# Performance work log

Measured on AMD Instinct MI355X. Metric: run time of the kernel, lower is better.

Reference implementation:

```python
import jax, jax.numpy as jnp
import numpy as np

B, H, S, D = 8, 32, 1024, 128
MAX_LEN = 2048
CACHE_POS = 128  # tokens already resident in cache (memory tokens)


def setup_inputs() -> dict:
    key = jax.random.key(0)
    k1, k2, k3, k4, k5 = jax.random.split(key, 5)
    return {
        "query_states": jax.random.normal(k1, (B, H, S, D), dtype=jnp.float32),
        "key_states": jax.random.normal(k2, (B, H, S, D), dtype=jnp.float32),
        "value_states": jax.random.normal(k3, (B, H, S, D), dtype=jnp.float32),
        "key_cache": jax.random.normal(k4, (B, H, MAX_LEN, D), dtype=jnp.float32),
        "value_cache": jax.random.normal(k5, (B, H, MAX_LEN, D), dtype=jnp.float32),
        "cache_position": CACHE_POS,
    }


def reference(query_states, key_states, value_states, key_cache, value_cache, cache_position):
    # --- HymbaCache.update_cache ---
    seq_len = key_states.shape[2]
    end_pos = cache_position + seq_len  # == sliding_window + num_memory_tokens, no shift needed
    key_cache = jax.lax.dynamic_update_slice(key_cache, key_states, (0, 0, cache_position, 0))
    value_cache = jax.lax.dynamic_update_slice(value_cache, value_states, (0, 0, cache_position, 0))
    k = key_cache[:, :, :end_pos]    # [B,H,end_pos,D]
    v = value_cache[:, :, :end_pos]  # [B,H,end_pos,D]
    # --- scaled dot-product attention over cached K/V ---
    scale = 1.0 / jnp.sqrt(jnp.asarray(k.shape[-1], dtype=query_states.dtype))
    scores = jnp.einsum('bhqd,bhkd->bhqk', query_states, k) * scale
    attn = jax.nn.softmax(scores, axis=-1)
    out = jnp.einsum('bhqk,bhkd->bhqd', attn, v)
    return out
```

## Files before the change

### kernel.cpp

```cpp
#include <hip/hip_runtime.h>
#include <hip/hip_bf16.h>
#include <stdint.h>

constexpr int Bb = 8, Hh = 32, Ss = 1024, Dd = 128, ML = 2048;
constexpr int CACHE_POS_C = 128;
constexpr int QT = 128;
constexpr int KT = 32;
constexpr int NTT = (CACHE_POS_C + Ss) / KT;
constexpr int PSTR = 40;

typedef __attribute__((ext_vector_type(8))) short bf16x8;
typedef __attribute__((ext_vector_type(4))) float f32x4;
typedef __attribute__((ext_vector_type(4))) unsigned u32x4;

__device__ __forceinline__ short f2bf(float x) {
    __hip_bfloat16 h = __float2bfloat16(x);
    return __builtin_bit_cast(short, h);
}

__device__ __forceinline__ float fast_exp2(float x) {
#if __has_builtin(__builtin_amdgcn_exp2f)
    return __builtin_amdgcn_exp2f(x);
#else
    return exp2f(x);
#endif
}

__device__ __forceinline__ void gll16(const void* g, void* l) {
    __builtin_amdgcn_global_load_lds(
        (const __attribute__((address_space(1))) unsigned int*)(uintptr_t)g,
        (__attribute__((address_space(3))) unsigned int*)(uintptr_t)l,
        16, 0, 0);
}

__global__ __launch_bounds__(256)
void prepack(const float* __restrict__ KN, const float* __restrict__ VN,
             const float* __restrict__ KC, const float* __restrict__ VC,
             const int* __restrict__ CPOS, short* __restrict__ KP,
             short* __restrict__ VP)
{
    const int blk = blockIdx.x;
    const int bh  = blk / NTT;
    const int t   = blk - bh * NTT;
    const int cpos = CPOS[0];
    const int endp = cpos + Ss;

    #pragma unroll
    for (int r = 0; r < 2; ++r) {
        const int c  = r * 256 + threadIdx.x;
        const int kk = c >> 7, h = (c >> 6) & 1, l = c & 63;
        const int row = t * KT + 2 * (l & 15) + h;
        const int d0  = kk * 32 + (l >> 4) * 8;
        bf16x8 o;
        if (row < endp) {
            const float* src = (row < cpos)
                ? KC + ((size_t)bh * ML + row) * Dd + d0
                : KN + ((size_t)bh * Ss + (row - cpos)) * Dd + d0;
            float4 a = ((const float4*)src)[0];
            float4 b = ((const float4*)src)[1];
            o[0] = f2bf(a.x); o[1] = f2bf(a.y); o[2] = f2bf(a.z); o[3] = f2bf(a.w);
            o[4] = f2bf(b.x); o[5] = f2bf(b.y); o[6] = f2bf(b.z); o[7] = f2bf(b.w);
        } else {
            #pragma unroll
            for (int j = 0; j < 8; ++j) o[j] = 0;
        }
        *(bf16x8*)(&KP[((size_t)blk * 512 + c) * 8]) = o;
    }
    #pragma unroll
    for (int r = 0; r < 2; ++r) {
        const int c  = r * 256 + threadIdx.x;
        const int tt = c >> 6, l = c & 63;
        const int d   = tt * 16 + (l & 15);
        const int kv0 = t * KT + (l >> 4) * 8;
        bf16x8 o;
        #pragma unroll
        for (int j = 0; j < 8; ++j) {
            const int row = kv0 + j;
            float x = 0.f;
            if (row < endp) {
                x = (row < cpos) ? VC[((size_t)bh * ML + row) * Dd + d]
                                 : VN[((size_t)bh * Ss + (row - cpos)) * Dd + d];
            }
            o[j] = f2bf(x);
        }
        *(bf16x8*)(&VP[((size_t)blk * 512 + c) * 8]) = o;
    }
}

__global__ __launch_bounds__(256, 3)
void attn_main(const float* __restrict__ Q, const short* __restrict__ KP,
               const short* __restrict__ VP, const int* __restrict__ CPOS,
               float* __restrict__ OUT)
{
    __shared__ __align__(16) short Kl[2][4096];
    __shared__ __align__(16) short Vl[2][4096];

    const int tid = threadIdx.x;
    const int wv  = tid >> 6;
    const int l64 = tid & 63;
    const int g   = l64 >> 4;
    const int ln  = l64 & 15;

    const int bid = blockIdx.x;
    const int bh  = ((bid & 7) << 5) | (bid >> 6);
    const int qt  = (bid >> 3) & 7;
    const int q0w = qt * QT + wv * 32;

    const int cpos = CPOS[0];
    const int endp = cpos + Ss;
    int ntile = (endp + KT - 1) / KT;
    if (ntile > NTT) ntile = NTT;
    const float nInv = (float)(ntile * KT - endp);

    const float SCALE2 = 0.08838834764831845f * 1.44269504088896340736f;

    bf16x8 qf[2][4];
    #pragma unroll
    for (int rb = 0; rb < 2; ++rb) {
        const float* qr = Q + ((size_t)bh * Ss + q0w + rb * 16 + ln) * Dd + g * 8;
        #pragma unroll
        for (int kk = 0; kk < 4; ++kk) {
            float4 a = *(const float4*)(qr + kk * 32);
            float4 b = *(const float4*)(qr + kk * 32 + 4);
            bf16x8 f;
            f[0] = f2bf(a.x * SCALE2); f[1] = f2bf(a.y * SCALE2);
            f[2] = f2bf(a.z * SCALE2); f[3] = f2bf(a.w * SCALE2);
            f[4] = f2bf(b.x * SCALE2); f[5] = f2bf(b.y * SCALE2);
            f[6] = f2bf(b.z * SCALE2); f[7] = f2bf(b.w * SCALE2);
            qf[rb][kk] = f;
        }
    }

    f32x4 O[2][8];
    #pragma unroll
    for (int rb = 0; rb < 2; ++rb)
        #pragma unroll
        for (int t = 0; t < 8; ++t) O[rb][t] = (f32x4){0.f, 0.f, 0.f, 0.f};
    f32x4 Lacc[2];
    Lacc[0] = (f32x4){0.f, 0.f, 0.f, 0.f};
    Lacc[1] = (f32x4){0.f, 0.f, 0.f, 0.f};

    const f32x4 ZZ = (f32x4){0.f, 0.f, 0.f, 0.f};

    bf16x8 ones;
    #pragma unroll
    for (int j = 0; j < 8; ++j) ones[j] = (short)0x3F80;

    const size_t kbase = (size_t)bh * NTT * 4096;

    #pragma unroll
    for (int r = 0; r < 2; ++r) {
        const int ch = r * 256 + tid;
        gll16(KP + kbase + (size_t)ch * 8, &Kl[0][(r * 256 + wv * 64) * 8]);
        gll16(VP + kbase + (size_t)ch * 8, &Vl[0][(r * 256 + wv * 64) * 8]);
    }
    __syncthreads();

    int cur = 0;
    for (int t = 0; t < ntile; ++t) {
        if (t + 1 < ntile) {
            const size_t toff = kbase + (size_t)(t + 1) * 4096;
            #pragma unroll
            for (int r = 0; r < 2; ++r) {
                const int ch = r * 256 + tid;
                gll16(KP + toff + (size_t)ch * 8, &Kl[cur ^ 1][(r * 256 + wv * 64) * 8]);
                gll16(VP + toff + (size_t)ch * 8, &Vl[cur ^ 1][(r * 256 + wv * 64) * 8]);
            }
        }
        const short* Kc = Kl[cur] + (size_t)l64 * 8;
        const short* Vc = Vl[cur] + (size_t)l64 * 8;

        f32x4 sc[2][2];
        #pragma unroll
        for (int h = 0; h < 2; ++h) {
            bf16x8 kf = *(const bf16x8*)(Kc + h * 512);
            sc[0][h] = __builtin_amdgcn_mfma_f32_16x16x32_bf16(kf, qf[0][0], ZZ, 0, 0, 0);
            sc[1][h] = __builtin_amdgcn_mfma_f32_16x16x32_bf16(kf, qf[1][0], ZZ, 0, 0, 0);
        }
        #pragma unroll
        for (int h = 0; h < 2; ++h) {
            bf16x8 kf = *(const bf16x8*)(Kc + (2 + h) * 512);
            sc[0][h] = __builtin_amdgcn_mfma_f32_16x16x32_bf16(kf, qf[0][1], sc[0][h], 0, 0, 0);
            sc[1][h] = __builtin_amdgcn_mfma_f32_16x16x32_bf16(kf, qf[1][1], sc[1][h], 0, 0, 0);
        }

        bf16x8 vf[8];
        #pragma unroll
        for (int tt = 0; tt < 8; ++tt) vf[tt] = *(const bf16x8*)(Vc + tt * 512);

        #pragma unroll
        for (int kk = 2; kk < 4; ++kk) {
            #pragma unroll
            for (int h = 0; h < 2; ++h) {
                bf16x8 kf = *(const bf16x8*)(Kc + (kk * 2 + h) * 512);
                sc[0][h] = __builtin_amdgcn_mfma_f32_16x16x32_bf16(kf, qf[0][kk], sc[0][h], 0, 0, 0);
                sc[1][h] = __builtin_amdgcn_mfma_f32_16x16x32_bf16(kf, qf[1][kk], sc[1][h], 0, 0, 0);
            }
        }

        bf16x8 af[2];
        #pragma unroll
        for (int rb = 0; rb < 2; ++rb) {
            u32x4 pk;
            #pragma unroll
            for (int r = 0; r < 4; ++r) {
                float p0 = fast_exp2(sc[rb][0][r]);
                float p1 = fast_exp2(sc[rb][1][r]);
                pk[r] = ((unsigned)(unsigned short)f2bf(p1) << 16)
                      |  (unsigned)(unsigned short)f2bf(p0);
            }
            af[rb] = __builtin_bit_cast(bf16x8, pk);
        }

        Lacc[0] = __builtin_amdgcn_mfma_f32_16x16x32_bf16(af[0], ones, Lacc[0], 0, 0, 0);
        Lacc[1] = __builtin_amdgcn_mfma_f32_16x16x32_bf16(af[1], ones, Lacc[1], 0, 0, 0);
        #pragma unroll
        for (int tt = 0; tt < 8; ++tt) {
            O[0][tt] = __builtin_amdgcn_mfma_f32_16x16x32_bf16(af[0], vf[tt], O[0][tt], 0, 0, 0);
            O[1][tt] = __builtin_amdgcn_mfma_f32_16x16x32_bf16(af[1], vf[tt], O[1][tt], 0, 0, 0);
        }

        __syncthreads();
        cur ^= 1;
    }

    #pragma unroll
    for (int rb = 0; rb < 2; ++rb) {
        f32x4 inv;
        #pragma unroll
        for (int r = 0; r < 4; ++r) inv[r] = 1.0f / (Lacc[rb][r] - nInv);
        float* ob = OUT + ((size_t)bh * Ss + q0w + rb * 16) * Dd;
        #pragma unroll
        for (int tt = 0; tt < 8; ++tt)
            #pragma unroll
            for (int r = 0; r < 4; ++r)
                ob[(g * 4 + r) * Dd + tt * 16 + ln] = O[rb][tt][r] * inv[r];
    }
}

constexpr int KSTR_FB = 132;
constexpr int VSTR_FB = 72;

__global__ __launch_bounds__(256, 3)
void attn_fwd_fb(const float* __restrict__ Q, const float* __restrict__ KN,
                 const float* __restrict__ VN, const float* __restrict__ KC,
                 const float* __restrict__ VC, const int* __restrict__ CPOS,
                 float* __restrict__ OUT)
{
    __shared__ __align__(16) short Klds[KT * KSTR_FB];
    __shared__ __align__(16) short Vt[Dd * VSTR_FB];
    __shared__ __align__(16) short Plds[4][16 * PSTR];

    const int tid = threadIdx.x;
    const int wv  = tid >> 6;
    const int g   = (tid >> 4) & 3;
    const int ln  = tid & 15;

    const int bid = blockIdx.x;
    const int bh  = ((bid & 7) << 5) | (bid >> 6);
    const int qt  = (bid >> 3) & 7;
    const int q0w = qt * QT + wv * 32;

    const int cpos  = CPOS[0];
    const int endp  = cpos + Ss;
    const int ntile = (endp + KT - 1) / KT;
    const float SCALE2 = 0.08838834764831845f * 1.44269504088896340736f;

    bf16x8 qf[2][4];
    #pragma unroll
    for (int rb = 0; rb < 2; ++rb) {
        const float* qr = Q + ((size_t)bh * Ss + q0w + rb * 16 + ln) * Dd + g * 8;
        #pragma unroll
        for (int kk = 0; kk < 4; ++kk) {
            float4 a = *(const float4*)(qr + kk * 32);
            float4 b = *(const float4*)(qr + kk * 32 + 4);
            bf16x8 f;
            f[0] = f2bf(a.x); f[1] = f2bf(a.y); f[2] = f2bf(a.z); f[3] = f2bf(a.w);
            f[4] = f2bf(b.x); f[5] = f2bf(b.y); f[6] = f2bf(b.z); f[7] = f2bf(b.w);
            qf[rb][kk] = f;
        }
    }

    f32x4 O[2][8];
    #pragma unroll
    for (int rb = 0; rb < 2; ++rb)
        #pragma unroll
        for (int t = 0; t < 8; ++t) O[rb][t] = (f32x4){0.f, 0.f, 0.f, 0.f};
    f32x4 Lacc[2];
    Lacc[0] = (f32x4){0.f, 0.f, 0.f, 0.f};
    Lacc[1] = (f32x4){0.f, 0.f, 0.f, 0.f};
    bf16x8 ones;
    #pragma unroll
    for (int j = 0; j < 8; ++j) ones[j] = (short)0x3F80;

    const int ksrow = tid >> 3;
    const int kscol = (tid & 7) * 16;
    const int vd    = tid & 127;
    const int vhalf = tid >> 7;

    for (int t = 0; t < ntile; ++t) {
        const int kv0 = t * KT;
        __syncthreads();
        {
            const int gkv = kv0 + ksrow;
            short kb[16];
            if (gkv < endp) {
                const float* ksrc = (gkv < cpos)
                    ? KC + ((size_t)bh * ML + gkv) * Dd + kscol
                    : KN + ((size_t)bh * Ss + (gkv - cpos)) * Dd + kscol;
                #pragma unroll
                for (int j = 0; j < 4; ++j) {
                    float4 k4 = ((const float4*)ksrc)[j];
                    kb[j*4+0] = f2bf(k4.x); kb[j*4+1] = f2bf(k4.y);
                    kb[j*4+2] = f2bf(k4.z); kb[j*4+3] = f2bf(k4.w);
                }
            } else {
                #pragma unroll
                for (int j = 0; j < 16; ++j) kb[j] = 0;
            }
            bf16x8 klo, khi;
            #pragma unroll
            for (int j = 0; j < 8; ++j) { klo[j] = kb[j]; khi[j] = kb[8+j]; }
            *(bf16x8*)(&Klds[ksrow * KSTR_FB + kscol])     = klo;
            *(bf16x8*)(&Klds[ksrow * KSTR_FB + kscol + 8]) = khi;
        }
        #pragma unroll
        for (int rblk = 0; rblk < 2; ++rblk) {
            const int r0 = vhalf * 16 + rblk * 8;
            bf16x8 vv;
            #pragma unroll
            for (int j = 0; j < 8; ++j) {
                const int row = kv0 + r0 + j;
                float x = 0.f;
                if (row < endp) {
                    x = (row < cpos) ? VC[((size_t)bh * ML + row) * Dd + vd]
                                     : VN[((size_t)bh * Ss + (row - cpos)) * Dd + vd];
                }
                vv[j] = f2bf(x);
            }
            *(bf16x8*)(&Vt[vd * VSTR_FB + r0]) = vv;
        }
        __syncthreads();

        f32x4 sc[2][2];
        #pragma unroll
        for (int rb = 0; rb < 2; ++rb)
            #pragma unroll
            for (int h = 0; h < 2; ++h) sc[rb][h] = (f32x4){0.f, 0.f, 0.f, 0.f};
        #pragma unroll
        for (int h = 0; h < 2; ++h) {
            #pragma unroll
            for (int kk = 0; kk < 4; ++kk) {
                bf16x8 kf = *(const bf16x8*)(&Klds[(2*ln + h) * KSTR_FB + kk*32 + g*8]);
                sc[0][h] = __builtin_amdgcn_mfma_f32_16x16x32_bf16(qf[0][kk], kf, sc[0][h], 0, 0, 0);
                sc[1][h] = __builtin_amdgcn_mfma_f32_16x16x32_bf16(qf[1][kk], kf, sc[1][h], 0, 0, 0);
            }
        }

        const bool v0 = (kv0 + 2*ln + 0) < endp;
        const bool v1 = (kv0 + 2*ln + 1) < endp;
        bf16x8 af[2];
        #pragma unroll
        for (int rb = 0; rb < 2; ++rb) {
            #pragma unroll
            for (int r = 0; r < 4; ++r) {
                float s0 = v0 ? sc[rb][0][r] * SCALE2 : -1e30f;
                float s1 = v1 ? sc[rb][1][r] * SCALE2 : -1e30f;
                s0 = fminf(s0, 30.f); s1 = fminf(s1, 30.f);
                float p0 = exp2f(s0);
                float p1 = exp2f(s1);
                unsigned pk = ((unsigned)(unsigned short)f2bf(p1) << 16)
                            |  (unsigned)(unsigned short)f2bf(p0);
                ((unsigned*)(&Plds[wv][0]))[(g*4 + r) * (PSTR/2) + ln] = pk;
            }
            af[rb] = *(const bf16x8*)(&Plds[wv][ln * PSTR + g * 8]);
            Lacc[rb] = __builtin_amdgcn_mfma_f32_16x16x32_bf16(af[rb], ones, Lacc[rb], 0, 0, 0);
        }

        #pragma unroll
        for (int tt = 0; tt < 8; ++tt) {
            bf16x8 vf = *(const bf16x8*)(&Vt[(tt*16 + ln) * VSTR_FB + g * 8]);
            O[0][tt] = __builtin_amdgcn_mfma_f32_16x16x32_bf16(af[0], vf, O[0][tt], 0, 0, 0);
            O[1][tt] = __builtin_amdgcn_mfma_f32_16x16x32_bf16(af[1], vf, O[1][tt], 0, 0, 0);
        }
    }

    #pragma unroll
    for (int rb = 0; rb < 2; ++rb) {
        f32x4 inv;
        #pragma unroll
        for (int r = 0; r < 4; ++r) inv[r] = 1.0f / Lacc[rb][r];
        float* ob = OUT + ((size_t)bh * Ss + q0w + rb * 16) * Dd;
        #pragma unroll
        for (int tt = 0; tt < 8; ++tt)
            #pragma unroll
            for (int r = 0; r < 4; ++r)
                ob[(g*4 + r) * Dd + tt*16 + ln] = O[rb][tt][r] * inv[r];
    }
}

extern "C" void kernel_launch(void* const* d_in, const int* in_sizes, int n_in,
                              void* d_out, int out_size, void* d_ws, size_t ws_size,
                              hipStream_t stream) {
    const float* Q  = (const float*)d_in[0];
    const float* KN = (const float*)d_in[1];
    const float* VN = (const float*)d_in[2];
    const float* KC = (const float*)d_in[3];
    const float* VC = (const float*)d_in[4];
    const int* CPOS = (const int*)d_in[5];
    float* OUT = (float*)d_out;

    const size_t per_buf = (size_t)(Bb * Hh) * NTT * 4096;
    const size_t need    = 2 * per_buf * sizeof(short);

    if (ws_size >= need) {
        short* KP = (short*)d_ws;
        short* VP = KP + per_buf;
        prepack<<<dim3(Bb * Hh * NTT), dim3(256), 0, stream>>>(KN, VN, KC, VC, CPOS, KP, VP);
        attn_main<<<dim3((Ss / QT) * Bb * Hh), dim3(256), 0, stream>>>(Q, KP, VP, CPOS, OUT);
    } else {
        attn_fwd_fb<<<dim3((Ss / QT) * Bb * Hh), dim3(256), 0, stream>>>(Q, KN, VN, KC, VC, CPOS, OUT);
    }
}
```

Before: 257.4 us.

## Double query rows per wave to reuse K/V tiles across more queries

Each wave now handles 64 query rows (four 16-row blocks) instead of 32, so a block covers 256 queries and each K/V tile loaded into LDS is reused by twice as many MFMAs. The grid halves to 1024 blocks, and occupancy drops to one block per CU via launch bounds, because the per-thread accumulators and Q fragments double. The softmax/PV work is split into two halves to limit live registers. This risks register pressure and less latency hiding in exchange for halving K/V LDS and global traffic per query.

```diff
diff --git a/kernel.cpp b/kernel.cpp
--- a/kernel.cpp
+++ b/kernel.cpp
@@ -4,7 +4,7 @@
 
 constexpr int Bb = 8, Hh = 32, Ss = 1024, Dd = 128, ML = 2048;
 constexpr int CACHE_POS_C = 128;
-constexpr int QT = 128;
+constexpr int QT = 256;
 constexpr int KT = 32;
 constexpr int NTT = (CACHE_POS_C + Ss) / KT;
 constexpr int PSTR = 40;
@@ -87,7 +87,7 @@
     }
 }
 
-__global__ __launch_bounds__(256, 3)
+__global__ __launch_bounds__(256, 1)
 void attn_main(const float* __restrict__ Q, const short* __restrict__ KP,
                const short* __restrict__ VP, const int* __restrict__ CPOS,
                float* __restrict__ OUT)
@@ -102,9 +102,9 @@
     const int ln  = l64 & 15;
 
     const int bid = blockIdx.x;
-    const int bh  = ((bid & 7) << 5) | (bid >> 6);
-    const int qt  = (bid >> 3) & 7;
-    const int q0w = qt * QT + wv * 32;
+    const int bh  = ((bid & 7) << 5) | (bid >> 5);
+    const int qt  = (bid >> 3) & 3;
+    const int q0w = qt * QT + wv * 64;
 
     const int cpos = CPOS[0];
     const int endp = cpos + Ss;
@@ -114,9 +114,9 @@
 
     const float SCALE2 = 0.08838834764831845f * 1.44269504088896340736f;
 
-    bf16x8 qf[2][4];
-    #pragma unroll
-    for (int rb = 0; rb < 2; ++rb) {
+    bf16x8 qf[4][4];
+    #pragma unroll
+    for (int rb = 0; rb < 4; ++rb) {
         const float* qr = Q + ((size_t)bh * Ss + q0w + rb * 16 + ln) * Dd + g * 8;
         #pragma unroll
         for (int kk = 0; kk < 4; ++kk) {
@@ -131,14 +131,14 @@
         }
     }
 
-    f32x4 O[2][8];
-    #pragma unroll
-    for (int rb = 0; rb < 2; ++rb)
+    f32x4 O[4][8];
+    #pragma unroll
+    for (int rb = 0; rb < 4; ++rb)
         #pragma unroll
         for (int t = 0; t < 8; ++t) O[rb][t] = (f32x4){0.f, 0.f, 0.f, 0.f};
-    f32x4 Lacc[2];
-    Lacc[0] = (f32x4){0.f, 0.f, 0.f, 0.f};
-    Lacc[1] = (f32x4){0.f, 0.f, 0.f, 0.f};
+    f32x4 Lacc[4];
+    #pragma unroll
+    for (int rb = 0; rb < 4; ++rb) Lacc[rb] = (f32x4){0.f, 0.f, 0.f, 0.f};
 
     const f32x4 ZZ = (f32x4){0.f, 0.f, 0.f, 0.f};
 
@@ -170,54 +170,70 @@
         const short* Kc = Kl[cur] + (size_t)l64 * 8;
         const short* Vc = Vl[cur] + (size_t)l64 * 8;
 
-        f32x4 sc[2][2];
+        f32x4 sc[4][2];
         #pragma unroll
         for (int h = 0; h < 2; ++h) {
             bf16x8 kf = *(const bf16x8*)(Kc + h * 512);
-            sc[0][h] = __builtin_amdgcn_mfma_f32_16x16x32_bf16(kf, qf[0][0], ZZ, 0, 0, 0);
-            sc[1][h] = __builtin_amdgcn_mfma_f32_16x16x32_bf16(kf, qf[1][0], ZZ, 0, 0, 0);
-        }
-        #pragma unroll
-        for (int h = 0; h < 2; ++h) {
-            bf16x8 kf = *(const bf16x8*)(Kc + (2 + h) * 512);
-            sc[0][h] = __builtin_amdgcn_mfma_f32_16x16x32_bf16(kf, qf[0][1], sc[0][h], 0, 0, 0);
-            sc[1][h] = __builtin_amdgcn_mfma_f32_16x16x32_bf16(kf, qf[1][1], sc[1][h], 0, 0, 0);
-        }
-
-        bf16x8 vf[8];
-        #pragma unroll
-        for (int tt = 0; tt < 8; ++tt) vf[tt] = *(const bf16x8*)(Vc + tt * 512);
-
-        #pragma unroll
-        for (int kk = 2; kk < 4; ++kk) {
+            #pragma unroll
+            for (int rb = 0; rb < 4; ++rb)
+                sc[rb][h] = __builtin_amdgcn_mfma_f32_16x16x32_bf16(kf, qf[rb][0], ZZ, 0, 0, 0);
+        }
+        #pragma unroll
+        for (int kk = 1; kk < 4; ++kk) {
             #pragma unroll
             for (int h = 0; h < 2; ++h) {
                 bf16x8 kf = *(const bf16x8*)(Kc + (kk * 2 + h) * 512);
-                sc[0][h] = __builtin_amdgcn_mfma_f32_16x16x32_bf16(kf, qf[0][kk], sc[0][h], 0, 0, 0);
-                sc[1][h] = __builtin_amdgcn_mfma_f32_16x16x32_bf16(kf, qf[1][kk], sc[1][h], 0, 0, 0);
-            }
-        }
-
-        bf16x8 af[2];
-        #pragma unroll
-        for (int rb = 0; rb < 2; ++rb) {
-            u32x4 pk;
+                #pragma unroll
+                for (int rb = 0; rb < 4; ++rb)
+                    sc[rb][h] = __builtin_amdgcn_mfma_f32_16x16x32_bf16(kf, qf[rb][kk], sc[rb][h], 0, 0, 0);
+            }
+        }
+
+        bf16x8 vf[8];
+        #pragma unroll
+        for (int tt = 0; tt < 8; ++tt) vf[tt] = *(const bf16x8*)(Vc + tt * 512);
+
+        bf16x8 af0, af1, af2, af3;
+        {
+            u32x4 pk0, pk1;
             #pragma unroll
             for (int r = 0; r < 4; ++r) {
-                float p0 = fast_exp2(sc[rb][0][r]);
-                float p1 = fast_exp2(sc[rb][1][r]);
-                pk[r] = ((unsigned)(unsigned short)f2bf(p1) << 16)
-                      |  (unsigned)(unsigned short)f2bf(p0);
-            }
-            af[rb] = __builtin_bit_cast(bf16x8, pk);
-        }
-
-        Lacc[0] = __builtin_amdgcn_mfma_f32_16x16x32_bf16(af[0], ones, Lacc[0], 0, 0, 0);
-        Lacc[1] = __builtin_amdgcn_mfma_f32_16x16x32_bf16(af[1], ones, Lacc[1], 0, 0, 0);
+                pk0[r] = ((unsigned)(unsigned short)f2bf(fast_exp2(sc[0][1][r])) << 16)
+                       |  (unsigned)(unsigned short)f2bf(fast_exp2(sc[0][0][r]));
+                pk1[r] = ((unsigned)(unsigned short)f2bf(fast_exp2(sc[1][1][r])) << 16)
+                       |  (unsigned)(unsigned short)f2bf(fast_exp2(sc[1][0][r]));
+            }
+            af0 = __builtin_bit_cast(bf16x8, pk0);
+            af1 = __builtin_bit_cast(bf16x8, pk1);
+        }
+
+        Lacc[0] = __builtin_amdgcn_mfma_f32_16x16x32_bf16(af0, ones, Lacc[0], 0, 0, 0);
+        Lacc[1] = __builtin_amdgcn_mfma_f32_16x16x32_bf16(af1, ones, Lacc[1], 0, 0, 0);
         #pragma unroll
         for (int tt = 0; tt < 8; ++tt) {
-            O[0][tt] = __builtin_amdgcn_mfma_f32_16x16x32_bf16(af[0], vf[tt], O[0][tt], 0, 0, 0);
-            O[1][tt] = __builtin_amdgcn_mfma_f32_16x16x32_bf16(af[1], vf[tt], O[1][tt], 0, 0, 0);
+            O[0][tt] = __builtin_amdgcn_mfma_f32_16x16x32_bf16(af0, vf[tt], O[0][tt], 0, 0, 0);
+            O[1][tt] = __builtin_amdgcn_mfma_f32_16x16x32_bf16(af1, vf[tt], O[1][tt], 0, 0, 0);
+        }
+
+        {
+            u32x4 pk2, pk3;
+            #pragma unroll
+            for (int r = 0; r < 4; ++r) {
+                pk2[r] = ((unsigned)(unsigned short)f2bf(fast_exp2(sc[2][1][r])) << 16)
+                       |  (unsigned)(unsigned short)f2bf(fast_exp2(sc[2][0][r]));
+                pk3[r] = ((unsigned)(unsigned short)f2bf(fast_exp2(sc[3][1][r])) << 16)
+                       |  (unsigned)(unsigned short)f2bf(fast_exp2(sc[3][0][r]));
+            }
+            af2 = __builtin_bit_cast(bf16x8, pk2);
+            af3 = __builtin_bit_cast(bf16x8, pk3);
+        }
+
+        Lacc[2] = __builtin_amdgcn_mfma_f32_16x16x32_bf16(af2, ones, Lacc[2], 0, 0, 0);
+        Lacc[3] = __builtin_amdgcn_mfma_f32_16x16x32_bf16(af3, ones, Lacc[3], 0, 0, 0);
+        #pragma unroll
+        for (int tt = 0; tt < 8; ++tt) {
+            O[2][tt] = __builtin_amdgcn_mfma_f32_16x16x32_bf16(af2, vf[tt], O[2][tt], 0, 0, 0);
+            O[3][tt] = __builtin_amdgcn_mfma_f32_16x16x32_bf16(af3, vf[tt], O[3][tt], 0, 0, 0);
         }
 
         __syncthreads();
@@ -225,7 +241,7 @@
     }
 
     #pragma unroll
-    for (int rb = 0; rb < 2; ++rb) {
+    for (int rb = 0; rb < 4; ++rb) {
         f32x4 inv;
         #pragma unroll
         for (int r = 0; r < 4; ++r) inv[r] = 1.0f / (Lacc[rb][r] - nInv);
@@ -240,6 +256,7 @@
 
 constexpr int KSTR_FB = 132;
 constexpr int VSTR_FB = 72;
+constexpr int QT_FB = 128;
 
 __global__ __launch_bounds__(256, 3)
 void attn_fwd_fb(const float* __restrict__ Q, const float* __restrict__ KN,
@@ -259,7 +276,7 @@
     const int bid = blockIdx.x;
     const int bh  = ((bid & 7) << 5) | (bid >> 6);
     const int qt  = (bid >> 3) & 7;
-    const int q0w = qt * QT + wv * 32;
+    const int q0w = qt * QT_FB + wv * 32;
 
     const int cpos  = CPOS[0];
     const int endp  = cpos + Ss;
@@ -419,6 +436,6 @@
         prepack<<<dim3(Bb * Hh * NTT), dim3(256), 0, stream>>>(KN, VN, KC, VC, CPOS, KP, VP);
         attn_main<<<dim3((Ss / QT) * Bb * Hh), dim3(256), 0, stream>>>(Q, KP, VP, CPOS, OUT);
     } else {
-        attn_fwd_fb<<<dim3((Ss / QT) * Bb * Hh), dim3(256), 0, stream>>>(Q, KN, VN, KC, VC, CPOS, OUT);
-    }
-}
+        attn_fwd_fb<<<dim3((Ss / QT_FB) * Bb * Hh), dim3(256), 0, stream>>>(Q, KN, VN, KC, VC, CPOS, OUT);
+    }
+}
```

Result: slower. 329.3 us (+27.9%).

## Software-pipeline attention loop so PV MFMAs overlap next tile's QK and exp

Applied to the files above, without the earlier changes.

Restructures the main attention loop into a prologue, steady state and epilogue. Each iteration now issues the P·V and row-sum MFMAs for the previous tile alongside the QK MFMAs for the current tile, then computes exp and loads V for the current tile before the barrier. The aim is to hide exp/convert latency and MFMA dependency stalls behind independent matrix work, at the cost of keeping extra registers live (the previous tile's P fragments and V fragments).

```diff
diff --git a/kernel.cpp b/kernel.cpp
--- a/kernel.cpp
+++ b/kernel.cpp
@@ -148,6 +148,9 @@
 
     const size_t kbase = (size_t)bh * NTT * 4096;
 
+    bf16x8 af0, af1;
+    bf16x8 vf[8];
+
     #pragma unroll
     for (int r = 0; r < 2; ++r) {
         const int ch = r * 256 + tid;
@@ -156,8 +159,51 @@
     }
     __syncthreads();
 
-    int cur = 0;
-    for (int t = 0; t < ntile; ++t) {
+    {
+        if (1 < ntile) {
+            const size_t toff = kbase + 4096;
+            #pragma unroll
+            for (int r = 0; r < 2; ++r) {
+                const int ch = r * 256 + tid;
+                gll16(KP + toff + (size_t)ch * 8, &Kl[1][(r * 256 + wv * 64) * 8]);
+                gll16(VP + toff + (size_t)ch * 8, &Vl[1][(r * 256 + wv * 64) * 8]);
+            }
+        }
+        const short* Kc = Kl[0] + (size_t)l64 * 8;
+        f32x4 sc[2][2];
+        #pragma unroll
+        for (int h = 0; h < 2; ++h) {
+            bf16x8 kf = *(const bf16x8*)(Kc + h * 512);
+            sc[0][h] = __builtin_amdgcn_mfma_f32_16x16x32_bf16(kf, qf[0][0], ZZ, 0, 0, 0);
+            sc[1][h] = __builtin_amdgcn_mfma_f32_16x16x32_bf16(kf, qf[1][0], ZZ, 0, 0, 0);
+        }
+        #pragma unroll
+        for (int kk = 1; kk < 4; ++kk) {
+            #pragma unroll
+            for (int h = 0; h < 2; ++h) {
+                bf16x8 kf = *(const bf16x8*)(Kc + (kk * 2 + h) * 512);
+                sc[0][h] = __builtin_amdgcn_mfma_f32_16x16x32_bf16(kf, qf[0][kk], sc[0][h], 0, 0, 0);
+                sc[1][h] = __builtin_amdgcn_mfma_f32_16x16x32_bf16(kf, qf[1][kk], sc[1][h], 0, 0, 0);
+            }
+        }
+        u32x4 pk0, pk1;
+        #pragma unroll
+        for (int r = 0; r < 4; ++r) {
+            pk0[r] = ((unsigned)(unsigned short)f2bf(fast_exp2(sc[0][1][r])) << 16)
+                   |  (unsigned)(unsigned short)f2bf(fast_exp2(sc[0][0][r]));
+            pk1[r] = ((unsigned)(unsigned short)f2bf(fast_exp2(sc[1][1][r])) << 16)
+                   |  (unsigned)(unsigned short)f2bf(fast_exp2(sc[1][0][r]));
+        }
+        af0 = __builtin_bit_cast(bf16x8, pk0);
+        af1 = __builtin_bit_cast(bf16x8, pk1);
+        const short* Vc = Vl[0] + (size_t)l64 * 8;
+        #pragma unroll
+        for (int tt = 0; tt < 8; ++tt) vf[tt] = *(const bf16x8*)(Vc + tt * 512);
+        __syncthreads();
+    }
+
+    int cur = 1;
+    for (int t = 1; t < ntile; ++t) {
         if (t + 1 < ntile) {
             const size_t toff = kbase + (size_t)(t + 1) * 4096;
             #pragma unroll
@@ -168,7 +214,6 @@
             }
         }
         const short* Kc = Kl[cur] + (size_t)l64 * 8;
-        const short* Vc = Vl[cur] + (size_t)l64 * 8;
 
         f32x4 sc[2][2];
         #pragma unroll
@@ -178,18 +223,7 @@
             sc[1][h] = __builtin_amdgcn_mfma_f32_16x16x32_bf16(kf, qf[1][0], ZZ, 0, 0, 0);
         }
         #pragma unroll
-        for (int h = 0; h < 2; ++h) {
-            bf16x8 kf = *(const bf16x8*)(Kc + (2 + h) * 512);
-            sc[0][h] = __builtin_amdgcn_mfma_f32_16x16x32_bf16(kf, qf[0][1], sc[0][h], 0, 0, 0);
-            sc[1][h] = __builtin_amdgcn_mfma_f32_16x16x32_bf16(kf, qf[1][1], sc[1][h], 0, 0, 0);
-        }
-
-        bf16x8 vf[8];
-        #pragma unroll
-        for (int tt = 0; tt < 8; ++tt) vf[tt] = *(const bf16x8*)(Vc + tt * 512);
-
-        #pragma unroll
-        for (int kk = 2; kk < 4; ++kk) {
+        for (int kk = 1; kk < 4; ++kk) {
             #pragma unroll
             for (int h = 0; h < 2; ++h) {
                 bf16x8 kf = *(const bf16x8*)(Kc + (kk * 2 + h) * 512);
@@ -198,32 +232,43 @@
             }
         }
 
-        bf16x8 af[2];
-        #pragma unroll
-        for (int rb = 0; rb < 2; ++rb) {
-            u32x4 pk;
+        Lacc[0] = __builtin_amdgcn_mfma_f32_16x16x32_bf16(af0, ones, Lacc[0], 0, 0, 0);
+        Lacc[1] = __builtin_amdgcn_mfma_f32_16x16x32_bf16(af1, ones, Lacc[1], 0, 0, 0);
+        #pragma unroll
+        for (int tt = 0; tt < 8; ++tt) {
+            O[0][tt] = __builtin_amdgcn_mfma_f32_16x16x32_bf16(af0, vf[tt], O[0][tt], 0, 0, 0);
+            O[1][tt] = __builtin_amdgcn_mfma_f32_16x16x32_bf16(af1, vf[tt], O[1][tt], 0, 0, 0);
+        }
+
+        {
+            u32x4 pk0, pk1;
             #pragma unroll
             for (int r = 0; r < 4; ++r) {
-                float p0 = fast_exp2(sc[rb][0][r]);
-                float p1 = fast_exp2(sc[rb][1][r]);
-                pk[r] = ((unsigned)(unsigned short)f2bf(p1) << 16)
-                      |  (unsigned)(unsigned short)f2bf(p0);
-            }
-            af[rb] = __builtin_bit_cast(bf16x8, pk);
-        }
-
-        Lacc[0] = __builtin_amdgcn_mfma_f32_16x16x32_bf16(af[0], ones, Lacc[0], 0, 0, 0);
-        Lacc[1] = __builtin_amdgcn_mfma_f32_16x16x32_bf16(af[1], ones, Lacc[1], 0, 0, 0);
-        #pragma unroll
-        for (int tt = 0; tt < 8; ++tt) {
-            O[0][tt] = __builtin_amdgcn_mfma_f32_16x16x32_bf16(af[0], vf[tt], O[0][tt], 0, 0, 0);
-            O[1][tt] = __builtin_amdgcn_mfma_f32_16x16x32_bf16(af[1], vf[tt], O[1][tt], 0, 0, 0);
-        }
+                pk0[r] = ((unsigned)(unsigned short)f2bf(fast_exp2(sc[0][1][r])) << 16)
+                       |  (unsigned)(unsigned short)f2bf(fast_exp2(sc[0][0][r]));
+                pk1[r] = ((unsigned)(unsigned short)f2bf(fast_exp2(sc[1][1][r])) << 16)
+                       |  (unsigned)(unsigned short)f2bf(fast_exp2(sc[1][0][r]));
+            }
+            af0 = __builtin_bit_cast(bf16x8, pk0);
+            af1 = __builtin_bit_cast(bf16x8, pk1);
+        }
+
+        const short* Vc = Vl[cur] + (size_t)l64 * 8;
+        #pragma unroll
+        for (int tt = 0; tt < 8; ++tt) vf[tt] = *(const bf16x8*)(Vc + tt * 512);
 
         __syncthreads();
         cur ^= 1;
     }
 
+    Lacc[0] = __builtin_amdgcn_mfma_f32_16x16x32_bf16(af0, ones, Lacc[0], 0, 0, 0);
+    Lacc[1] = __builtin_amdgcn_mfma_f32_16x16x32_bf16(af1, ones, Lacc[1], 0, 0, 0);
+    #pragma unroll
+    for (int tt = 0; tt < 8; ++tt) {
+        O[0][tt] = __builtin_amdgcn_mfma_f32_16x16x32_bf16(af0, vf[tt], O[0][tt], 0, 0, 0);
+        O[1][tt] = __builtin_amdgcn_mfma_f32_16x16x32_bf16(af1, vf[tt], O[1][tt], 0, 0, 0);
+    }
+
     #pragma unroll
     for (int rb = 0; rb < 2; ++rb) {
         f32x4 inv;
@@ -240,6 +285,7 @@
 
 constexpr int KSTR_FB = 132;
 constexpr int VSTR_FB = 72;
+constexpr int QT_FB = 128;
 
 __global__ __launch_bounds__(256, 3)
 void attn_fwd_fb(const float* __restrict__ Q, const float* __restrict__ KN,
@@ -259,7 +305,7 @@
     const int bid = blockIdx.x;
     const int bh  = ((bid & 7) << 5) | (bid >> 6);
     const int qt  = (bid >> 3) & 7;
-    const int q0w = qt * QT + wv * 32;
+    const int q0w = qt * QT_FB + wv * 32;
 
     const int cpos  = CPOS[0];
     const int endp  = cpos + Ss;
@@ -419,6 +465,6 @@
         prepack<<<dim3(Bb * Hh * NTT), dim3(256), 0, stream>>>(KN, VN, KC, VC, CPOS, KP, VP);
         attn_main<<<dim3((Ss / QT) * Bb * Hh), dim3(256), 0, stream>>>(Q, KP, VP, CPOS, OUT);
     } else {
-        attn_fwd_fb<<<dim3((Ss / QT) * Bb * Hh), dim3(256), 0, stream>>>(Q, KN, VN, KC, VC, CPOS, OUT);
-    }
-}
+        attn_fwd_fb<<<dim3((Ss / QT_FB) * Bb * Hh), dim3(256), 0, stream>>>(Q, KN, VN, KC, VC, CPOS, OUT);
+    }
+}
```

Result: slower. 350.1 us (+36.0%).
